# Performance work log

Measured on AMD Instinct MI355X. Metric: run time of the kernel, lower is better.

The kernel has to match this reference:

```python
import jax, jax.numpy as jnp
import numpy as np

N, E = 3200, 50000
RBF, HID = 16, 128
CUT = 5.0
NS, NV = 32, 16            # multiplicities of 0e and 1o blocks
D = NS + 3 * NV            # 80 = node/message irrep dim
WNUM = NS*NS + NV*NS + NS*NV + NV*NV  # 2304 tensor-product weights per edge
EPS = 1e-8
# path normalization (fully-connected TP, 2 paths per output irrep)
A1 = 1.0 / np.sqrt(2.0 * NS)
A2 = 1.0 / np.sqrt(2.0 * NV)
A3 = 1.0 / np.sqrt(2.0 * NS)
A4 = 1.0 / np.sqrt(2.0 * NV)
ISQ3 = 1.0 / np.sqrt(3.0)


def setup_inputs() -> dict:
    key = jax.random.key(0)
    ks = jax.random.split(key, 24)
    nrm = lambda k, s, sc=1.0: jax.random.normal(k, s, jnp.float32) * sc
    x = nrm(ks[0], (N, D))
    edge_src = jax.random.randint(ks[1], (E,), 0, N)
    edge_dst = jax.random.randint(ks[2], (E,), 0, N)
    dirs = nrm(ks[3], (E, 3))
    unit = dirs / jnp.linalg.norm(dirs, axis=1, keepdims=True)
    # component-normalized SH for l=0,1: [1, sqrt(3)*r_hat]
    edge_sh = jnp.concatenate([jnp.ones((E, 1), jnp.float32), np.sqrt(3.0) * unit], axis=1)
    edge_rbf = nrm(ks[4], (E, RBF))
    edge_len = jax.random.uniform(ks[5], (E,), jnp.float32, 0.1, 6.0)  # some beyond cutoff
    inp = dict(x=x, edge_src=edge_src, edge_dst=edge_dst, edge_sh=edge_sh,
               edge_rbf=edge_rbf, edge_len=edge_len)
    # IrrepNorm affine params
    inp['norm_w'] = jnp.ones((D,), jnp.float32)
    inp['norm_b'] = jnp.zeros((D,), jnp.float32)
    # radial weight MLP (RBF -> HID -> HID -> WNUM)
    inp['mw1'] = nrm(ks[6], (RBF, HID), 1.0/np.sqrt(RBF)); inp['mb1'] = jnp.zeros((HID,), jnp.float32)
    inp['mw2'] = nrm(ks[7], (HID, HID), 1.0/np.sqrt(HID)); inp['mb2'] = jnp.zeros((HID,), jnp.float32)
    inp['mw3'] = nrm(ks[8], (HID, WNUM), 1.0/np.sqrt(HID)); inp['mb3'] = jnp.zeros((WNUM,), jnp.float32)
    # edge gate MLP (RBF -> HID -> 1)
    inp['gw1'] = nrm(ks[9], (RBF, HID), 1.0/np.sqrt(RBF)); inp['gb1'] = jnp.zeros((HID,), jnp.float32)
    inp['gw2'] = nrm(ks[10], (HID, 1), 1.0/np.sqrt(HID)); inp['gb2'] = jnp.zeros((1,), jnp.float32)
    # equivariant linears (e3nn stores N(0,1) weights, normalizes by 1/sqrt(fan_in))
    inp['Ws'] = nrm(ks[11], (NS, NS + NV))   # msg_linear scalar part: 32 -> 32 scalars + 16 gates
    inp['Wv'] = nrm(ks[12], (NV, NV))        # msg_linear vector part
    inp['Us'] = nrm(ks[13], (NS, NS))        # update_linear
    inp['Uv'] = nrm(ks[14], (NV, NV))
    inp['Ss'] = nrm(ks[15], (NS, NS))        # self_linear
    inp['Sv'] = nrm(ks[16], (NV, NV))
    inp['res_scale'] = jnp.float32(0.1)
    return inp


def _irrep_norm(x, w, b):
    s = x[:, :NS]
    v = x[:, NS:].reshape(-1, NV, 3)
    mean = s.mean(axis=1, keepdims=True)
    var = ((s - mean) ** 2).mean(axis=1, keepdims=True)
    s = (s - mean) / jnp.sqrt(var + EPS)
    rms = jnp.sqrt((v ** 2).mean(axis=2, keepdims=True) + EPS)
    v = v / rms
    out = jnp.concatenate([s, v.reshape(-1, 3 * NV)], axis=-1)
    return out * w + b


def reference(x, edge_src, edge_dst, edge_sh, edge_rbf, edge_len,
              norm_w, norm_b, mw1, mb1, mw2, mb2, mw3, mb3,
              gw1, gb1, gw2, gb2, Ws, Wv, Us, Uv, Ss, Sv, res_scale):
    silu = jax.nn.silu
    x_norm = _irrep_norm(x, norm_w, norm_b)                  # [N, 80]
    # radial tensor-product weights per edge
    h = silu(edge_rbf @ mw1 + mb1)
    h = silu(h @ mw2 + mb2)
    tpw = h @ mw3 + mb3                                      # [E, 2304]
    o1 = NS*NS; o2 = o1 + NV*NS; o3 = o2 + NS*NV
    w1 = tpw[:, :o1].reshape(-1, NS, NS)
    w2 = tpw[:, o1:o2].reshape(-1, NV, NS)
    w3 = tpw[:, o2:o3].reshape(-1, NS, NV)
    w4 = tpw[:, o3:].reshape(-1, NV, NV)
    # gather source node features
    xs = x_norm[edge_src, :NS]                               # [E, 32]
    xv = x_norm[edge_src, NS:].reshape(-1, NV, 3)            # [E, 16, 3]
    sh0 = edge_sh[:, 0]                                      # [E]
    sh1 = edge_sh[:, 1:4]                                    # [E, 3]
    # fully-connected TP paths
    msg_s = A1 * jnp.einsum('ei,eio->eo', xs * sh0[:, None], w1)
    inner = jnp.einsum('eim,em->ei', xv, sh1) * ISQ3         # 1o x 1o -> 0e
    msg_s = msg_s + A2 * jnp.einsum('ei,eio->eo', inner, w2)
    msg_v = A3 * jnp.einsum('ei,eio->eo', xs, w3)[:, :, None] * sh1[:, None, :]
    msg_v = msg_v + A4 * jnp.einsum('eim,eio->eom', xv, w4) * sh0[:, None, None]
    m = jnp.concatenate([msg_s, msg_v.reshape(-1, 3 * NV)], axis=-1)  # [E, 80]
    # cutoff envelope and learned edge gate
    cutoff_w = 0.5 * (jnp.cos(jnp.pi * edge_len / CUT) + 1.0) * (edge_len <= CUT).astype(x.dtype)
    gate_w = jax.nn.sigmoid(silu(edge_rbf @ gw1 + gb1) @ gw2 + gb2)   # [E, 1]
    edge_w = cutoff_w[:, None] * gate_w                               # [E, 1]
    m = m * edge_w
    # scatter-add aggregate + normalization
    agg = jax.ops.segment_sum(m, edge_dst, num_segments=N)            # [N, 80]
    den = jax.ops.segment_sum(edge_w, edge_dst, num_segments=N)       # [N, 1]
    agg = agg / jnp.maximum(den, 1e-8)
    # msg_linear -> scalars + gates + gated vectors
    ag_s = agg[:, :NS]
    ag_v = agg[:, NS:].reshape(-1, NV, 3)
    sc = (ag_s @ Ws) / np.sqrt(NS)                                    # [N, 48]
    vc = jnp.einsum('nim,io->nom', ag_v, Wv) / np.sqrt(NV)            # [N, 16, 3]
    s_g = silu(sc[:, :NS])
    gates = jax.nn.sigmoid(sc[:, NS:])
    v_g = vc * gates[:, :, None]
    # update + self interaction
    upd_s = (s_g @ Us) / np.sqrt(NS)
    upd_v = jnp.einsum('nim,io->nom', v_g, Uv) / np.sqrt(NV)
    self_s = (x_norm[:, :NS] @ Ss) / np.sqrt(NS)
    self_v = jnp.einsum('nim,io->nom', x_norm[:, NS:].reshape(-1, NV, 3), Sv) / np.sqrt(NV)
    out = jnp.concatenate([self_s + upd_s, (self_v + upd_v).reshape(-1, 3 * NV)], axis=-1)
    return x + res_scale * out
```

## Files before the change

### kernel.cpp

```cpp
#include <hip/hip_runtime.h>
#include <hip/hip_bf16.h>
#include <math.h>

#define N_NODES 3200
#define E_EDGES 50000
#define RBFN 16
#define HID 128
#define NS 32
#define NV 16
#define DD 80
#define WNUM 2304
#define CUTF 5.0f
#define EPSF 1e-8f

#define A1C 0.125f
#define A2C 0.17677669529663687f
#define A3C 0.125f
#define A4C 0.17677669529663687f
#define A2ISQ 0.10206207261596575f

typedef __attribute__((ext_vector_type(4))) float f32x4;
typedef __attribute__((ext_vector_type(8))) short bf16x8;

__device__ __forceinline__ float sigm(float x) { return 1.0f / (1.0f + __expf(-x)); }
__device__ __forceinline__ float silu_f(float x) { return x * sigm(x); }

__device__ __forceinline__ short bf16r(float x) {
    union { float f; unsigned u; } v; v.f = x;
    unsigned r = (v.u + 0x7fffu + ((v.u >> 16) & 1u)) >> 16;
    return (short)r;
}
__device__ __forceinline__ float b2f(unsigned short s) {
    union { float f; unsigned u; } v; v.u = ((unsigned)s) << 16; return v.f;
}

__global__ void k_scan(const int* __restrict__ hist, int* __restrict__ start) {
    __shared__ int part[256];
    int t = threadIdx.x;
    int loc[13];
    int s = 0;
#pragma unroll
    for (int j = 0; j < 13; j++) {
        int idx = t * 13 + j;
        int v = (idx < N_NODES) ? hist[idx] : 0;
        loc[j] = s; s += v;
    }
    part[t] = s;
    __syncthreads();
    for (int off = 1; off < 256; off <<= 1) {
        int v = part[t];
        int add = (t >= off) ? part[t - off] : 0;
        __syncthreads();
        part[t] = v + add;
        __syncthreads();
    }
    int pre = (t == 0) ? 0 : part[t - 1];
#pragma unroll
    for (int j = 0; j < 13; j++) {
        int idx = t * 13 + j;
        if (idx < N_NODES) start[idx] = pre + loc[j];
    }
    if (t == 255) start[N_NODES] = part[255];
}

__global__ void k_scatter(const int* __restrict__ edst, const int* __restrict__ start,
                          int* __restrict__ cur, int* __restrict__ perm) {
    int e = blockIdx.x * 256 + threadIdx.x;
    if (e < E_EDGES) {
        int d = edst[e];
        int pos = start[d] + atomicAdd(&cur[d], 1);
        perm[pos] = e;
    }
}

__global__ void k_prep0(const float* __restrict__ mw2, __hip_bfloat16* __restrict__ mw2f) {
    __shared__ __hip_bfloat16 st[2048];
    int t = blockIdx.x, tid = threadIdx.x;
    for (int idx = tid; idx < 2048; idx += 256) {
        int k = idx >> 4, c = idx & 15;
        float v = mw2[k * HID + t * 16 + c];
        int kk = k >> 5, q4 = (k >> 3) & 3, j = k & 7;
        st[kk * 512 + (q4 * 16 + c) * 8 + j] = __float2bfloat16(v);
    }
    __syncthreads();
    ((bf16x8*)(mw2f + t * 2048))[tid] = ((const bf16x8*)st)[tid];
}

__global__ __launch_bounds__(256) void k_front(
    const float* __restrict__ rbf, const float* __restrict__ elen,
    const int* __restrict__ edst,
    const float* __restrict__ mw1, const float* __restrict__ mb1,
    const float* __restrict__ gw1, const float* __restrict__ gb1,
    const float* __restrict__ gw2, const float* __restrict__ gb2,
    const float* __restrict__ mb2, const __hip_bfloat16* __restrict__ mw2f,
    const float* __restrict__ mw3, const float* __restrict__ mb3,
    const float* __restrict__ x, const float* __restrict__ nw, const float* __restrict__ nb,
    float* __restrict__ ewg, __hip_bfloat16* __restrict__ h2b,
    __hip_bfloat16* __restrict__ mw3f, __hip_bfloat16* __restrict__ biasf,
    float* __restrict__ xn, int* __restrict__ hist) {
    __shared__ __align__(16) char smem[16640];
    int b = blockIdx.x, tid = threadIdx.x;
    if (b < 782) {
        __hip_bfloat16* h1l = (__hip_bfloat16*)smem;
        int wid = __builtin_amdgcn_readfirstlane(tid >> 6);
        int lane = tid & 63;
        int base = b * 64;
        int eb = base + wid * 16;
        {
            int c0 = lane, c1 = 64 + lane;
            float t0[16], t1[16], g0[16], g1[16];
            float b0 = mb1[c0], b1 = mb1[c1], gb0v = gb1[c0], gb1v = gb1[c1];
#pragma unroll
            for (int e = 0; e < 16; e++) { t0[e] = b0; t1[e] = b1; g0[e] = gb0v; g1[e] = gb1v; }
#pragma unroll
            for (int r = 0; r < RBFN; r++) {
                float w0 = mw1[r * HID + c0], w1 = mw1[r * HID + c1];
                float v0 = gw1[r * HID + c0], v1 = gw1[r * HID + c1];
#pragma unroll
                for (int e = 0; e < 16; e++) {
                    int ee = eb + e; if (ee >= E_EDGES) ee = E_EDGES - 1;
                    float rv = rbf[ee * RBFN + r];
                    t0[e] += rv * w0; t1[e] += rv * w1;
                    g0[e] += rv * v0; g1[e] += rv * v1;
                }
            }
            float q0 = gw2[c0], q1 = gw2[c1];
            float gb2v = gb2[0];
#pragma unroll
            for (int e = 0; e < 16; e++) {
                int le = wid * 16 + e;
                h1l[le * 128 + c0] = __float2bfloat16(silu_f(t0[e]));
                h1l[le * 128 + c1] = __float2bfloat16(silu_f(t1[e]));
                float p = silu_f(g0[e]) * q0 + silu_f(g1[e]) * q1;
                p += __shfl_xor(p, 1);  p += __shfl_xor(p, 2);  p += __shfl_xor(p, 4);
                p += __shfl_xor(p, 8);  p += __shfl_xor(p, 16); p += __shfl_xor(p, 32);
                if (lane == 0 && eb + e < E_EDGES) {
                    float len = elen[eb + e];
                    float cut = (len <= CUTF) ? 0.5f * (cosf(3.14159265358979f * len / CUTF) + 1.0f) : 0.f;
                    ewg[eb + e] = cut * sigm(p + gb2v);
                }
            }
        }
        __syncthreads();
        {
            int q4 = lane >> 4, l15 = lane & 15;
            int le = wid * 16 + l15;
            bf16x8 af[4];
#pragma unroll
            for (int kk = 0; kk < 4; kk++)
                af[kk] = *(const bf16x8*)(h1l + le * 128 + kk * 32 + q4 * 8);
            const f32x4 zf = {0.f, 0.f, 0.f, 0.f};
#pragma unroll
            for (int ct = 0; ct < 8; ct++) {
                f32x4 acc = zf;
#pragma unroll
                for (int kk = 0; kk < 4; kk++) {
                    bf16x8 bw = *(const bf16x8*)(mw2f + (ct * 4 + kk) * 512 + lane * 8);
                    acc = __builtin_amdgcn_mfma_f32_16x16x32_bf16(af[kk], bw, acc, 0, 0, 0);
                }
                float bias = mb2[ct * 16 + l15];
#pragma unroll
                for (int r = 0; r < 4; r++) {
                    int ge = base + wid * 16 + q4 * 4 + r;
                    if (ge < E_EDGES)
                        h2b[ge * HID + ct * 16 + l15] = __float2bfloat16(silu_f(acc[r] + bias));
                }
            }
        }
    } else if (b < 927) {
        int b2 = b - 782;
        __hip_bfloat16* st = (__hip_bfloat16*)smem;
        if (b2 < 144) {
            for (int idx = tid; idx < 2048; idx += 256) {
                int k = idx >> 4, c = idx & 15;
                float v = mw3[k * WNUM + b2 * 16 + c];
                int kk = k >> 5, q4 = (k >> 3) & 3, j = k & 7;
                st[kk * 512 + (q4 * 16 + c) * 8 + j] = __float2bfloat16(v);
            }
            __syncthreads();
            ((bf16x8*)(mw3f + b2 * 2048))[tid] = ((const bf16x8*)st)[tid];
        } else {
            for (int idx = tid; idx < 3072; idx += 256) {
                float val;
                if (idx < 1024) {
                    int oh = idx >> 9, l = (idx >> 3) & 63, j = idx & 7;
                    int o = oh * 16 + (l & 15), i = (l >> 4) * 8 + j;
                    val = mb3[i * 32 + o];
                } else if (idx < 2048) {
                    int t = idx - 1024;
                    int oh = t >> 9, l = (t >> 3) & 63, j = t & 7;
                    int o = oh * 16 + (l & 15), i = (l >> 4) * 8 + j;
                    val = (i < 16) ? mb3[1024 + i * 32 + o] : 0.f;
                } else if (idx < 2560) {
                    int t = idx - 2048;
                    int l = t >> 3, j = t & 7;
                    int o = l & 15, i = (l >> 4) * 8 + j;
                    val = mb3[1536 + i * 16 + o];
                } else {
                    int t = idx - 2560;
                    int l = t >> 3, j = t & 7;
                    int o = l & 15, i = (l >> 4) * 8 + j;
                    val = (i < 16) ? mb3[2048 + i * 16 + o] : 0.f;
                }
                biasf[idx] = __float2bfloat16(val);
            }
        }
    } else if (b < 1727) {
        float* row = (float*)smem;
        int sub = tid >> 6, t = tid & 63;
        int n = (b - 927) * 4 + sub;
        float* rw = row + sub * 80;
        const float* xr = x + n * DD;
        rw[t] = xr[t];
        if (t < 16) rw[64 + t] = xr[64 + t];
        __syncthreads();
        float mean = 0.f;
#pragma unroll
        for (int i = 0; i < NS; i++) mean += rw[i];
        mean *= (1.0f / NS);
        float var = 0.f;
#pragma unroll
        for (int i = 0; i < NS; i++) { float d = rw[i] - mean; var += d * d; }
        var *= (1.0f / NS);
        float inv = rsqrtf(var + EPSF);
        if (t < NS) xn[n * DD + t] = (rw[t] - mean) * inv * nw[t] + nb[t];
        if (t < 48) {
            int j = t / 3;
            float v0 = rw[NS + 3 * j], v1 = rw[NS + 3 * j + 1], v2 = rw[NS + 3 * j + 2];
            float rms = sqrtf((v0 * v0 + v1 * v1 + v2 * v2) * (1.0f / 3.0f) + EPSF);
            xn[n * DD + NS + t] = rw[NS + t] / rms * nw[NS + t] + nb[NS + t];
        }
    } else {
        int e = (b - 1727) * 256 + tid;
        if (e < E_EDGES) atomicAdd(&hist[edst[e]], 1);
    }
}

__global__ __launch_bounds__(128, 3) void k_msg(
    const float* __restrict__ xn, const __hip_bfloat16* __restrict__ h2b,
    const float* __restrict__ ewg, const int* __restrict__ esrc,
    const int* __restrict__ edst, const int* __restrict__ perm,
    const float* __restrict__ esh,
    const __hip_bfloat16* __restrict__ mw3f, const __hip_bfloat16* __restrict__ biasf,
    const int* __restrict__ startp, float* __restrict__ agg, float* __restrict__ agg2,
    float* __restrict__ den) {
    __shared__ __align__(16) char pool[29696];
    unsigned short (*xng)[82]  = (unsigned short(*)[82])(pool);
    unsigned short (*innr)[16] = (unsigned short(*)[16])(pool + 20992);
    float* sh0l = (float*)(pool + 25088);
    int* srcl   = (int*)(pool + 25600);
    int* gel    = (int*)(pool + 26112);
    int* dstl   = (int*)(pool + 26624);
    float* ewl  = (float*)(pool + 27136);
    float (*sh1l)[4] = (float(*)[4])(pool + 27648);
    float* msgl = (float*)pool;

    const int tid = threadIdx.x;
    const int wid = __builtin_amdgcn_readfirstlane(tid >> 6);
    const int lane = tid & 63;
    const int q4 = lane >> 4;
    const int l15 = lane & 15;
    const int ib = q4 * 8;
    const int grp = blockIdx.x / 5;
    const int slice = blockIdx.x - 5 * grp;
    const int e0 = grp * 128;

    {
        int slot = e0 + tid;
        bool v = slot < E_EDGES;
        int ge = v ? perm[slot] : 0;
        gel[tid] = ge;
        srcl[tid] = esrc[ge];
        dstl[tid] = v ? edst[ge] : -1;
        ewl[tid] = v ? ewg[ge] : 0.f;
        sh0l[tid] = esh[ge * 4];
        sh1l[tid][0] = esh[ge * 4 + 1];
        sh1l[tid][1] = esh[ge * 4 + 2];
        sh1l[tid][2] = esh[ge * 4 + 3];
    }
    __syncthreads();
    {
        int lo, hi;
        if (slice < 2)      { lo = 0;  hi = 32; }
        else if (slice < 4) { lo = 24; hi = 80; }
        else                { lo = 0;  hi = 80; }
        int nv4 = (hi - lo) >> 2;
        for (int idx = tid; idx < 128 * nv4; idx += 128) {
            int e = idx / nv4, k = idx - e * nv4;
            int q = lo + (k << 2);
            f32x4 v = *(const f32x4*)(xn + srcl[e] * 80 + q);
            unsigned p0 = ((unsigned)(unsigned short)bf16r(v[0])) |
                          (((unsigned)(unsigned short)bf16r(v[1])) << 16);
            unsigned p1 = ((unsigned)(unsigned short)bf16r(v[2])) |
                          (((unsigned)(unsigned short)bf16r(v[3])) << 16);
            unsigned* d = (unsigned*)&xng[e][q];
            d[0] = p0; d[1] = p1;
        }
    }
    __syncthreads();
    if (slice == 2 || slice == 3) {
        for (int idx = tid; idx < 128 * 16; idx += 128) {
            int e = idx >> 4, i = idx & 15;
            float d = b2f(xng[e][32 + 3 * i]) * sh1l[e][0]
                    + b2f(xng[e][32 + 3 * i + 1]) * sh1l[e][1]
                    + b2f(xng[e][32 + 3 * i + 2]) * sh1l[e][2];
            innr[e][i] = (unsigned short)bf16r(A2ISQ * d);
        }
        __syncthreads();
    }

    int el[4];
#pragma unroll
    for (int et = 0; et < 4; et++) el[et] = wid * 64 + et * 16 + l15;
    bf16x8 hfr[4][4];
#pragma unroll
    for (int et = 0; et < 4; et++) {
        int ge = gel[el[et]];
        const __hip_bfloat16* hr = h2b + ge * HID;
#pragma unroll
        for (int kk = 0; kk < 4; kk++)
            hfr[et][kk] = *(const bf16x8*)(hr + kk * 32 + ib);
    }
    const f32x4 zf = {0.f, 0.f, 0.f, 0.f};
    const bf16x8* gp = (const bf16x8*)mw3f;
    int cnt = E_EDGES - e0; if (cnt > 128) cnt = 128;

    if (slice < 4) {
        const int h = slice & 1;
        const int ch2 = slice >> 1;
        const int nlo = ch2 * 24, nhi = nlo + 24;
        float f1[4];
        f32x4 msgS[4];
#pragma unroll
        for (int et = 0; et < 4; et++) f1[et] = A1C * sh0l[el[et]];
#pragma unroll
        for (int et = 0; et < 4; et++) {
            bf16x8 pb;
            if (ch2 == 0) {
#pragma unroll
                for (int j = 0; j < 8; j++)
                    pb[j] = bf16r(b2f(xng[el[et]][ib + j]) * f1[et]);
            } else {
#pragma unroll
                for (int j = 0; j < 8; j++)
                    pb[j] = (ib + j < 16) ? (short)innr[el[et]][ib + j] : (short)0;
            }
            bf16x8 ba = *(const bf16x8*)(biasf + (ch2 * 1024 + h * 512) + lane * 8);
            msgS[et] = __builtin_amdgcn_mfma_f32_16x16x32_bf16(ba, pb, zf, 0, 0, 0);
        }
        auto computeS = [&](int n, bf16x8 (&A)[4]) {
            f32x4 acc[4];
#pragma unroll
            for (int et = 0; et < 4; et++) acc[et] = zf;
#pragma unroll
            for (int kk = 0; kk < 4; kk++)
#pragma unroll
                for (int et = 0; et < 4; et++)
                    acc[et] = __builtin_amdgcn_mfma_f32_16x16x32_bf16(
                        A[kk], hfr[et][kk], acc[et], 0, 0, 0);
            float p[4];
            if (n < 32) {
#pragma unroll
                for (int et = 0; et < 4; et++) p[et] = f1[et] * b2f(xng[el[et]][n]);
            } else {
#pragma unroll
                for (int et = 0; et < 4; et++) p[et] = b2f(innr[el[et]][n - 32]);
            }
#pragma unroll
            for (int et = 0; et < 4; et++)
#pragma unroll
                for (int r = 0; r < 4; r++)
                    msgS[et][r] += p[et] * acc[et][r];
        };
        bf16x8 A0[4], A1[4];
        {
            const bf16x8* g = gp + nlo * 512 + h * 256;
#pragma unroll
            for (int f = 0; f < 4; f++) A0[f] = g[f * 64 + lane];
        }
        for (int n = nlo; n < nhi; n += 2) {
            const bf16x8* g1 = gp + (n + 1) * 512 + h * 256;
#pragma unroll
            for (int f = 0; f < 4; f++) A1[f] = g1[f * 64 + lane];
            computeS(n, A0);
            if (n + 2 < nhi) {
                const bf16x8* g2 = gp + (n + 2) * 512 + h * 256;
#pragma unroll
                for (int f = 0; f < 4; f++) A0[f] = g2[f * 64 + lane];
            }
            computeS(n + 1, A1);
        }
        __syncthreads();
#pragma unroll
        for (int et = 0; et < 4; et++) {
            int le = el[et];
            float ew = ewl[le];
#pragma unroll
            for (int r = 0; r < 4; r++)
                msgl[le * 16 + q4 * 4 + r] = msgS[et][r] * ew;
        }
        __syncthreads();
        {
            int nch = (slice == 0) ? 17 : 16;
            int c = lane;
            int r0 = wid * 64;
            int rend = (cnt < r0 + 64) ? cnt : (r0 + 64);
            if (c < nch && r0 < cnt) {
                int cur = dstl[r0];
                float acc = 0.f;
                for (int r = r0; r < rend; r++) {
                    int nd = dstl[r];
                    if (nd != cur) {
                        if (cur >= 0) {
                            bool interior = (startp[cur] >= e0 + r0) && (startp[cur + 1] <= e0 + rend);
                            float* p = (c == 16) ? (den + cur)
                                     : ((slice == 0) ? (agg + cur * 80 + c)
                                     :  (slice == 1) ? (agg + cur * 80 + 16 + c)
                                     :  (slice == 2) ? (agg2 + cur * 32 + c)
                                                     : (agg2 + cur * 32 + 16 + c));
                            if (interior) *p = acc; else atomicAdd(p, acc);
                        }
                        acc = 0.f; cur = nd;
                    }
                    acc += (c == 16) ? ewl[r] : msgl[r * 16 + c];
                }
                if (cur >= 0) {
                    bool interior = (startp[cur] >= e0 + r0) && (startp[cur + 1] <= e0 + rend);
                    float* p = (c == 16) ? (den + cur)
                             : ((slice == 0) ? (agg + cur * 80 + c)
                             :  (slice == 1) ? (agg + cur * 80 + 16 + c)
                             :  (slice == 2) ? (agg2 + cur * 32 + c)
                                             : (agg2 + cur * 32 + 16 + c));
                    if (interior) *p = acc; else atomicAdd(p, acc);
                }
            }
        }
    } else {
        float f4e[4];
#pragma unroll
        for (int et = 0; et < 4; et++) f4e[et] = A4C * sh0l[el[et]];
        f32x4 q3[4];
#pragma unroll
        for (int et = 0; et < 4; et++) {
            bf16x8 xs8;
#pragma unroll
            for (int j = 0; j < 8; j++) xs8[j] = (short)xng[el[et]][ib + j];
            bf16x8 ba3 = *(const bf16x8*)(biasf + 2048 + lane * 8);
            q3[et] = __builtin_amdgcn_mfma_f32_16x16x32_bf16(ba3, xs8, zf, 0, 0, 0);
        }
        for (int n = 48; n < 64; ++n) {
            bf16x8 A[8];
            const bf16x8* g = gp + n * 512;
#pragma unroll
            for (int f = 0; f < 8; f++) A[f] = g[f * 64 + lane];
#pragma unroll
            for (int half = 0; half < 2; half++) {
                f32x4 acc[4];
#pragma unroll
                for (int et = 0; et < 4; et++) acc[et] = zf;
#pragma unroll
                for (int kk = 0; kk < 4; kk++)
#pragma unroll
                    for (int et = 0; et < 4; et++)
                        acc[et] = __builtin_amdgcn_mfma_f32_16x16x32_bf16(
                            A[half * 4 + kk], hfr[et][kk], acc[et], 0, 0, 0);
                int i = 2 * (n - 48) + half;
                float p[4];
#pragma unroll
                for (int et = 0; et < 4; et++) p[et] = b2f(xng[el[et]][i]);
#pragma unroll
                for (int et = 0; et < 4; et++)
#pragma unroll
                    for (int r = 0; r < 4; r++)
                        q3[et][r] += p[et] * acc[et][r];
            }
        }
        f32x4 qv[3][4];
#pragma unroll
        for (int et = 0; et < 4; et++) {
            bf16x8 ba4 = *(const bf16x8*)(biasf + 2560 + lane * 8);
#pragma unroll
            for (int m = 0; m < 3; m++) {
                bf16x8 t8;
#pragma unroll
                for (int j = 0; j < 8; j++) {
                    int i = ib + j;
                    t8[j] = (i < 16) ? (short)xng[el[et]][32 + 3 * i + m] : (short)0;
                }
                qv[m][et] = __builtin_amdgcn_mfma_f32_16x16x32_bf16(ba4, t8, zf, 0, 0, 0);
            }
        }
        for (int n = 64; n < 72; ++n) {
            bf16x8 A[8];
            const bf16x8* g = gp + n * 512;
#pragma unroll
            for (int f = 0; f < 8; f++) A[f] = g[f * 64 + lane];
#pragma unroll
            for (int half = 0; half < 2; half++) {
                f32x4 acc[4];
#pragma unroll
                for (int et = 0; et < 4; et++) acc[et] = zf;
#pragma unroll
                for (int kk = 0; kk < 4; kk++)
#pragma unroll
                    for (int et = 0; et < 4; et++)
                        acc[et] = __builtin_amdgcn_mfma_f32_16x16x32_bf16(
                            A[half * 4 + kk], hfr[et][kk], acc[et], 0, 0, 0);
                int i = 2 * (n - 64) + half;
#pragma unroll
                for (int m = 0; m < 3; m++) {
                    float p[4];
#pragma unroll
                    for (int et = 0; et < 4; et++) p[et] = b2f(xng[el[et]][32 + 3 * i + m]);
#pragma unroll
                    for (int et = 0; et < 4; et++)
#pragma unroll
                        for (int r = 0; r < 4; r++)
                            qv[m][et][r] += p[et] * acc[et][r];
                }
            }
        }
        __syncthreads();
#pragma unroll
        for (int et = 0; et < 4; et++) {
            int le = el[et];
            float ew = ewl[le];
            float s0 = sh1l[le][0], s1 = sh1l[le][1], s2 = sh1l[le][2];
            float b4 = f4e[et];
#pragma unroll
            for (int r = 0; r < 4; r++) {
                int o = q4 * 4 + r;
                float qq = A3C * q3[et][r];
                msgl[le * 48 + o * 3 + 0] = (qq * s0 + b4 * qv[0][et][r]) * ew;
                msgl[le * 48 + o * 3 + 1] = (qq * s1 + b4 * qv[1][et][r]) * ew;
                msgl[le * 48 + o * 3 + 2] = (qq * s2 + b4 * qv[2][et][r]) * ew;
            }
        }
        __syncthreads();
        {
            int c = lane;
            int r0 = wid * 64;
            int rend = (cnt < r0 + 64) ? cnt : (r0 + 64);
            if (c < 48 && r0 < cnt) {
                int cur = dstl[r0];
                float acc = 0.f;
                for (int r = r0; r < rend; r++) {
                    int nd = dstl[r];
                    if (nd != cur) {
                        if (cur >= 0) {
                            bool interior = (startp[cur] >= e0 + r0) && (startp[cur + 1] <= e0 + rend);
                            float* p = agg + cur * 80 + 32 + c;
                            if (interior) *p = acc; else atomicAdd(p, acc);
                        }
                        acc = 0.f; cur = nd;
                    }
                    acc += msgl[r * 48 + c];
                }
                if (cur >= 0) {
                    bool interior = (startp[cur] >= e0 + r0) && (startp[cur + 1] <= e0 + rend);
                    float* p = agg + cur * 80 + 32 + c;
                    if (interior) *p = acc; else atomicAdd(p, acc);
                }
            }
        }
    }
}

__global__ void k_update(
    const float* __restrict__ x, const float* __restrict__ xn,
    const float* __restrict__ agg, const float* __restrict__ agg2,
    const float* __restrict__ den,
    const float* __restrict__ Ws, const float* __restrict__ Wv,
    const float* __restrict__ Us, const float* __restrict__ Uv,
    const float* __restrict__ Ss, const float* __restrict__ Sv,
    const float* __restrict__ rsp, float* __restrict__ out) {
    int n = blockIdx.x, t = threadIdx.x;
    __shared__ float ag[DD];
    __shared__ float xnl[DD];
    __shared__ float sg[NS];
    __shared__ float gt[NV];
    __shared__ float vg[48];
    float idv = 1.0f / fmaxf(den[n], 1e-8f);
    float base = agg[n * DD + t];
    if (t < 32) base += agg2[n * 32 + t];
    ag[t] = base * idv;
    if (t < 16) ag[64 + t] = agg[n * DD + 64 + t] * idv;
    xnl[t] = xn[n * DD + t];
    if (t < 16) xnl[64 + t] = xn[n * DD + 64 + t];
    __syncthreads();
    const float iqs = 0.17677669529663687f;
    const float iqv = 0.25f;
    if (t < 48) {
        float acc = 0.f;
#pragma unroll
        for (int i = 0; i < NS; i++) acc += ag[i] * Ws[i * 48 + t];
        acc *= iqs;
        if (t < NS) sg[t] = silu_f(acc);
        else gt[t - NS] = sigm(acc);
    }
    __syncthreads();
    if (t < 48) {
        int o = t / 3, m = t - 3 * o;
        float acc = 0.f;
#pragma unroll
        for (int i = 0; i < NV; i++) acc += ag[NS + 3 * i + m] * Wv[i * NV + o];
        vg[t] = acc * iqv * gt[o];
    }
    __syncthreads();
    float rs = rsp[0];
    if (t < NS) {
        float us = 0.f, ss = 0.f;
#pragma unroll
        for (int i = 0; i < NS; i++) { us += sg[i] * Us[i * NS + t]; ss += xnl[i] * Ss[i * NS + t]; }
        out[n * DD + t] = x[n * DD + t] + rs * ((ss + us) * iqs);
    }
    if (t < 48) {
        int o = t / 3, m = t - 3 * o;
        float uv = 0.f, sv = 0.f;
#pragma unroll
        for (int i = 0; i < NV; i++) { uv += vg[3 * i + m] * Uv[i * NV + o]; sv += xnl[NS + 3 * i + m] * Sv[i * NV + o]; }
        out[n * DD + NS + t] = x[n * DD + NS + t] + rs * ((sv + uv) * iqv);
    }
}

extern "C" void kernel_launch(void* const* d_in, const int* in_sizes, int n_in,
                              void* d_out, int out_size, void* d_ws, size_t ws_size,
                              hipStream_t stream) {
    (void)in_sizes; (void)n_in; (void)out_size; (void)ws_size;
    const float* x    = (const float*)d_in[0];
    const int*   esrc = (const int*)d_in[1];
    const int*   edst = (const int*)d_in[2];
    const float* esh  = (const float*)d_in[3];
    const float* erbf = (const float*)d_in[4];
    const float* elen = (const float*)d_in[5];
    const float* nw   = (const float*)d_in[6];
    const float* nb   = (const float*)d_in[7];
    const float* mw1  = (const float*)d_in[8];
    const float* mb1  = (const float*)d_in[9];
    const float* mw2  = (const float*)d_in[10];
    const float* mb2  = (const float*)d_in[11];
    const float* mw3  = (const float*)d_in[12];
    const float* mb3  = (const float*)d_in[13];
    const float* gw1  = (const float*)d_in[14];
    const float* gb1  = (const float*)d_in[15];
    const float* gw2  = (const float*)d_in[16];
    const float* gb2  = (const float*)d_in[17];
    const float* Ws   = (const float*)d_in[18];
    const float* Wv   = (const float*)d_in[19];
    const float* Us   = (const float*)d_in[20];
    const float* Uv   = (const float*)d_in[21];
    const float* Ss   = (const float*)d_in[22];
    const float* Sv   = (const float*)d_in[23];
    const float* rsp  = (const float*)d_in[24];
    float* out = (float*)d_out;
    float* ws  = (float*)d_ws;

    float* agg    = ws;
    float* den    = ws + 256000;
    int*   hist   = (int*)(ws + 259200);
    int*   cur    = (int*)(ws + 262400);
    int*   startp = (int*)(ws + 265600);
    int*   perm   = (int*)(ws + 268801);
    float* xn     = ws + 318804;
    float* ewg    = ws + 574804;
    __hip_bfloat16* h2b   = (__hip_bfloat16*)(ws + 624804);
    __hip_bfloat16* mw3f  = (__hip_bfloat16*)(ws + 3824804);
    __hip_bfloat16* biasf = (__hip_bfloat16*)(ws + 3972260);
    __hip_bfloat16* mw2f  = (__hip_bfloat16*)(ws + 3973796);
    float* agg2   = ws + 3981988;

    hipMemsetAsync(ws, 0, 265600 * sizeof(float), stream);
    hipMemsetAsync(agg2, 0, 102400 * sizeof(float), stream);
    k_prep0<<<8, 256, 0, stream>>>(mw2, mw2f);
    k_front<<<1923, 256, 0, stream>>>(erbf, elen, edst, mw1, mb1, gw1, gb1, gw2, gb2,
                                      mb2, mw2f, mw3, mb3, x, nw, nb,
                                      ewg, h2b, mw3f, biasf, xn, hist);
    k_scan<<<1, 256, 0, stream>>>(hist, startp);
    k_scatter<<<196, 256, 0, stream>>>(edst, startp, cur, perm);
    k_msg<<<1955, 128, 0, stream>>>(xn, h2b, ewg, esrc, edst, perm, esh,
                                    mw3f, biasf, startp, agg, agg2, den);
    k_update<<<N_NODES, 64, 0, stream>>>(x, xn, agg, agg2, den, Ws, Wv, Us, Uv, Ss, Sv, rsp, out);
}
```

Before: 262.9 us.

## Pre-permute edge data by destination and store h2 in MFMA-tiled layout

The CSR build (histogram, scan, scatter) now runs before the front kernel. The scatter writes dst, src and sh arrays already in sorted order along with an inverse permutation. The front kernel writes edge weights and the h2 activations directly into sorted positions, with h2 in a 16-edge tiled layout that matches the MFMA fragment loads in the message kernel. It also emits a bf16 copy of the normalized node features, so the message kernel loads them with 16-byte vector reads instead of converting from fp32. This removes the gather through perm and the fp32→bf16 conversion from the hot message kernel. The cost is scattered writes in the front kernel, a serialized CSR build ahead of the front kernel, and launch bounds loosened from 3 to 2 blocks per unit, which may reduce occupancy.

```diff
diff --git a/kernel.cpp b/kernel.cpp
--- a/kernel.cpp
+++ b/kernel.cpp
@@ -34,6 +34,11 @@
     union { float f; unsigned u; } v; v.u = ((unsigned)s) << 16; return v.f;
 }
 
+__global__ void k_hist(const int* __restrict__ edst, int* __restrict__ hist) {
+    int e = blockIdx.x * 256 + threadIdx.x;
+    if (e < E_EDGES) atomicAdd(&hist[edst[e]], 1);
+}
+
 __global__ void k_scan(const int* __restrict__ hist, int* __restrict__ start) {
     __shared__ int part[256];
     int t = threadIdx.x;
@@ -63,13 +68,20 @@
     if (t == 255) start[N_NODES] = part[255];
 }
 
-__global__ void k_scatter(const int* __restrict__ edst, const int* __restrict__ start,
-                          int* __restrict__ cur, int* __restrict__ perm) {
+__global__ void k_scatter(const int* __restrict__ edst, const int* __restrict__ esrc,
+                          const float* __restrict__ esh, const int* __restrict__ start,
+                          int* __restrict__ cur, int* __restrict__ inv,
+                          int* __restrict__ edstp, int* __restrict__ esrcp,
+                          float* __restrict__ eshp) {
     int e = blockIdx.x * 256 + threadIdx.x;
     if (e < E_EDGES) {
         int d = edst[e];
         int pos = start[d] + atomicAdd(&cur[d], 1);
-        perm[pos] = e;
+        inv[e] = pos;
+        edstp[pos] = d;
+        esrcp[pos] = esrc[e];
+        f32x4 s = *(const f32x4*)(esh + e * 4);
+        *(f32x4*)(eshp + pos * 4) = s;
     }
 }
 
@@ -88,20 +100,21 @@
 
 __global__ __launch_bounds__(256) void k_front(
     const float* __restrict__ rbf, const float* __restrict__ elen,
-    const int* __restrict__ edst,
+    const int* __restrict__ inv,
     const float* __restrict__ mw1, const float* __restrict__ mb1,
     const float* __restrict__ gw1, const float* __restrict__ gb1,
     const float* __restrict__ gw2, const float* __restrict__ gb2,
     const float* __restrict__ mb2, const __hip_bfloat16* __restrict__ mw2f,
     const float* __restrict__ mw3, const float* __restrict__ mb3,
     const float* __restrict__ x, const float* __restrict__ nw, const float* __restrict__ nb,
-    float* __restrict__ ewg, __hip_bfloat16* __restrict__ h2b,
+    float* __restrict__ ewg, unsigned short* __restrict__ h2p,
     __hip_bfloat16* __restrict__ mw3f, __hip_bfloat16* __restrict__ biasf,
-    float* __restrict__ xn, int* __restrict__ hist) {
+    float* __restrict__ xn, unsigned short* __restrict__ xnb) {
     __shared__ __align__(16) char smem[16640];
     int b = blockIdx.x, tid = threadIdx.x;
     if (b < 782) {
         __hip_bfloat16* h1l = (__hip_bfloat16*)smem;
+        float* gatep = (float*)(smem + 16384);
         int wid = __builtin_amdgcn_readfirstlane(tid >> 6);
         int lane = tid & 63;
         int base = b * 64;
@@ -134,14 +147,18 @@
                 float p = silu_f(g0[e]) * q0 + silu_f(g1[e]) * q1;
                 p += __shfl_xor(p, 1);  p += __shfl_xor(p, 2);  p += __shfl_xor(p, 4);
                 p += __shfl_xor(p, 8);  p += __shfl_xor(p, 16); p += __shfl_xor(p, 32);
-                if (lane == 0 && eb + e < E_EDGES) {
-                    float len = elen[eb + e];
-                    float cut = (len <= CUTF) ? 0.5f * (cosf(3.14159265358979f * len / CUTF) + 1.0f) : 0.f;
-                    ewg[eb + e] = cut * sigm(p + gb2v);
-                }
-            }
-        }
-        __syncthreads();
+                if (lane == 0) gatep[le] = p + gb2v;
+            }
+        }
+        __syncthreads();
+        if (lane < 16) {
+            int ee = eb + lane;
+            if (ee < E_EDGES) {
+                float len = elen[ee];
+                float cut = (len <= CUTF) ? 0.5f * (cosf(3.14159265358979f * len / CUTF) + 1.0f) : 0.f;
+                ewg[inv[ee]] = cut * sigm(gatep[wid * 16 + lane]);
+            }
+        }
         {
             int q4 = lane >> 4, l15 = lane & 15;
             int le = wid * 16 + l15;
@@ -149,6 +166,12 @@
 #pragma unroll
             for (int kk = 0; kk < 4; kk++)
                 af[kk] = *(const bf16x8*)(h1l + le * 128 + kk * 32 + q4 * 8);
+            int pos4[4];
+#pragma unroll
+            for (int r = 0; r < 4; r++) {
+                int ge = base + wid * 16 + q4 * 4 + r;
+                pos4[r] = (ge < E_EDGES) ? inv[ge] : -1;
+            }
             const f32x4 zf = {0.f, 0.f, 0.f, 0.f};
 #pragma unroll
             for (int ct = 0; ct < 8; ct++) {
@@ -159,11 +182,14 @@
                     acc = __builtin_amdgcn_mfma_f32_16x16x32_bf16(af[kk], bw, acc, 0, 0, 0);
                 }
                 float bias = mb2[ct * 16 + l15];
+                int c = ct * 16 + l15;
+                int f = c >> 3, j = c & 7;
 #pragma unroll
                 for (int r = 0; r < 4; r++) {
-                    int ge = base + wid * 16 + q4 * 4 + r;
-                    if (ge < E_EDGES)
-                        h2b[ge * HID + ct * 16 + l15] = __float2bfloat16(silu_f(acc[r] + bias));
+                    int pos = pos4[r];
+                    if (pos >= 0)
+                        h2p[(pos >> 4) * 2048 + f * 128 + (pos & 15) * 8 + j] =
+                            (unsigned short)bf16r(silu_f(acc[r] + bias));
                 }
             }
         }
@@ -205,7 +231,7 @@
                 biasf[idx] = __float2bfloat16(val);
             }
         }
-    } else if (b < 1727) {
+    } else {
         float* row = (float*)smem;
         int sub = tid >> 6, t = tid & 63;
         int n = (b - 927) * 4 + sub;
@@ -222,37 +248,38 @@
 #pragma unroll
         for (int i = 0; i < NS; i++) { float d = rw[i] - mean; var += d * d; }
         var *= (1.0f / NS);
-        float inv = rsqrtf(var + EPSF);
-        if (t < NS) xn[n * DD + t] = (rw[t] - mean) * inv * nw[t] + nb[t];
+        float inv_ = rsqrtf(var + EPSF);
+        if (t < NS) {
+            float v = (rw[t] - mean) * inv_ * nw[t] + nb[t];
+            xn[n * DD + t] = v;
+            xnb[n * DD + t] = (unsigned short)bf16r(v);
+        }
         if (t < 48) {
             int j = t / 3;
             float v0 = rw[NS + 3 * j], v1 = rw[NS + 3 * j + 1], v2 = rw[NS + 3 * j + 2];
             float rms = sqrtf((v0 * v0 + v1 * v1 + v2 * v2) * (1.0f / 3.0f) + EPSF);
-            xn[n * DD + NS + t] = rw[NS + t] / rms * nw[NS + t] + nb[NS + t];
-        }
-    } else {
-        int e = (b - 1727) * 256 + tid;
-        if (e < E_EDGES) atomicAdd(&hist[edst[e]], 1);
-    }
-}
-
-__global__ __launch_bounds__(128, 3) void k_msg(
-    const float* __restrict__ xn, const __hip_bfloat16* __restrict__ h2b,
-    const float* __restrict__ ewg, const int* __restrict__ esrc,
-    const int* __restrict__ edst, const int* __restrict__ perm,
-    const float* __restrict__ esh,
+            float v = rw[NS + t] / rms * nw[NS + t] + nb[NS + t];
+            xn[n * DD + NS + t] = v;
+            xnb[n * DD + NS + t] = (unsigned short)bf16r(v);
+        }
+    }
+}
+
+__global__ __launch_bounds__(128, 2) void k_msg(
+    const unsigned short* __restrict__ xnb, const unsigned short* __restrict__ h2p,
+    const float* __restrict__ ewg, const int* __restrict__ edstp,
+    const int* __restrict__ esrcp, const float* __restrict__ eshp,
     const __hip_bfloat16* __restrict__ mw3f, const __hip_bfloat16* __restrict__ biasf,
     const int* __restrict__ startp, float* __restrict__ agg, float* __restrict__ agg2,
     float* __restrict__ den) {
-    __shared__ __align__(16) char pool[29696];
-    unsigned short (*xng)[82]  = (unsigned short(*)[82])(pool);
-    unsigned short (*innr)[16] = (unsigned short(*)[16])(pool + 20992);
-    float* sh0l = (float*)(pool + 25088);
-    int* srcl   = (int*)(pool + 25600);
-    int* gel    = (int*)(pool + 26112);
-    int* dstl   = (int*)(pool + 26624);
-    float* ewl  = (float*)(pool + 27136);
-    float (*sh1l)[4] = (float(*)[4])(pool + 27648);
+    __shared__ __align__(16) char pool[30720];
+    unsigned short (*xng)[88]  = (unsigned short(*)[88])(pool);
+    unsigned short (*innr)[16] = (unsigned short(*)[16])(pool + 22528);
+    float* sh0l = (float*)(pool + 26624);
+    int* srcl   = (int*)(pool + 27136);
+    int* dstl   = (int*)(pool + 27648);
+    float* ewl  = (float*)(pool + 28160);
+    float (*sh1l)[4] = (float(*)[4])(pool + 28672);
     float* msgl = (float*)pool;
 
     const int tid = threadIdx.x;
@@ -268,33 +295,29 @@
     {
         int slot = e0 + tid;
         bool v = slot < E_EDGES;
-        int ge = v ? perm[slot] : 0;
-        gel[tid] = ge;
-        srcl[tid] = esrc[ge];
-        dstl[tid] = v ? edst[ge] : -1;
-        ewl[tid] = v ? ewg[ge] : 0.f;
-        sh0l[tid] = esh[ge * 4];
-        sh1l[tid][0] = esh[ge * 4 + 1];
-        sh1l[tid][1] = esh[ge * 4 + 2];
-        sh1l[tid][2] = esh[ge * 4 + 3];
+        dstl[tid] = v ? edstp[slot] : -1;
+        srcl[tid] = v ? esrcp[slot] : 0;
+        ewl[tid]  = v ? ewg[slot] : 0.f;
+        f32x4 s = {0.f, 0.f, 0.f, 0.f};
+        if (v) s = *(const f32x4*)(eshp + slot * 4);
+        sh0l[tid] = s[0];
+        sh1l[tid][0] = s[1]; sh1l[tid][1] = s[2]; sh1l[tid][2] = s[3];
     }
     __syncthreads();
-    {
-        int lo, hi;
-        if (slice < 2)      { lo = 0;  hi = 32; }
-        else if (slice < 4) { lo = 24; hi = 80; }
-        else                { lo = 0;  hi = 80; }
-        int nv4 = (hi - lo) >> 2;
-        for (int idx = tid; idx < 128 * nv4; idx += 128) {
-            int e = idx / nv4, k = idx - e * nv4;
-            int q = lo + (k << 2);
-            f32x4 v = *(const f32x4*)(xn + srcl[e] * 80 + q);
-            unsigned p0 = ((unsigned)(unsigned short)bf16r(v[0])) |
-                          (((unsigned)(unsigned short)bf16r(v[1])) << 16);
-            unsigned p1 = ((unsigned)(unsigned short)bf16r(v[2])) |
-                          (((unsigned)(unsigned short)bf16r(v[3])) << 16);
-            unsigned* d = (unsigned*)&xng[e][q];
-            d[0] = p0; d[1] = p1;
+    if (slice < 2) {
+        for (int idx = tid; idx < 128 * 4; idx += 128) {
+            int e = idx >> 2, q = (idx & 3) * 8;
+            *(bf16x8*)&xng[e][q] = *(const bf16x8*)(xnb + srcl[e] * 80 + q);
+        }
+    } else if (slice < 4) {
+        for (int idx = tid; idx < 128 * 7; idx += 128) {
+            int e = idx / 7, q = 24 + (idx - e * 7) * 8;
+            *(bf16x8*)&xng[e][q] = *(const bf16x8*)(xnb + srcl[e] * 80 + q);
+        }
+    } else {
+        for (int idx = tid; idx < 128 * 10; idx += 128) {
+            int e = idx / 10, q = (idx - e * 10) * 8;
+            *(bf16x8*)&xng[e][q] = *(const bf16x8*)(xnb + srcl[e] * 80 + q);
         }
     }
     __syncthreads();
@@ -312,14 +335,14 @@
     int el[4];
 #pragma unroll
     for (int et = 0; et < 4; et++) el[et] = wid * 64 + et * 16 + l15;
+    const int tbase = (e0 >> 4) + wid * 4;
     bf16x8 hfr[4][4];
 #pragma unroll
     for (int et = 0; et < 4; et++) {
-        int ge = gel[el[et]];
-        const __hip_bfloat16* hr = h2b + ge * HID;
+        const unsigned short* tp = h2p + (tbase + et) * 2048;
 #pragma unroll
         for (int kk = 0; kk < 4; kk++)
-            hfr[et][kk] = *(const bf16x8*)(hr + kk * 32 + ib);
+            hfr[et][kk] = *(const bf16x8*)(tp + (kk * 4 + q4) * 128 + l15 * 8);
     }
     const f32x4 zf = {0.f, 0.f, 0.f, 0.f};
     const bf16x8* gp = (const bf16x8*)mw3f;
@@ -660,24 +683,30 @@
     int*   hist   = (int*)(ws + 259200);
     int*   cur    = (int*)(ws + 262400);
     int*   startp = (int*)(ws + 265600);
-    int*   perm   = (int*)(ws + 268801);
+    int*   inv    = (int*)(ws + 268801);
     float* xn     = ws + 318804;
     float* ewg    = ws + 574804;
-    __hip_bfloat16* h2b   = (__hip_bfloat16*)(ws + 624804);
-    __hip_bfloat16* mw3f  = (__hip_bfloat16*)(ws + 3824804);
-    __hip_bfloat16* biasf = (__hip_bfloat16*)(ws + 3972260);
-    __hip_bfloat16* mw2f  = (__hip_bfloat16*)(ws + 3973796);
-    float* agg2   = ws + 3981988;
+    unsigned short* h2p = (unsigned short*)(ws + 624804);
+    __hip_bfloat16* mw3f  = (__hip_bfloat16*)(ws + 3827876);
+    __hip_bfloat16* biasf = (__hip_bfloat16*)(ws + 3975332);
+    __hip_bfloat16* mw2f  = (__hip_bfloat16*)(ws + 3976868);
+    float* agg2   = ws + 3985060;
+    int* edstp    = (int*)(ws + 4087460);
+    int* esrcp    = (int*)(ws + 4137508);
+    float* eshp   = ws + 4187556;
+    unsigned short* xnb = (unsigned short*)(ws + 4387748);
 
     hipMemsetAsync(ws, 0, 265600 * sizeof(float), stream);
     hipMemsetAsync(agg2, 0, 102400 * sizeof(float), stream);
+    k_hist<<<196, 256, 0, stream>>>(edst, hist);
+    k_scan<<<1, 256, 0, stream>>>(hist, startp);
+    k_scatter<<<196, 256, 0, stream>>>(edst, esrc, esh, startp, cur,
+                                       inv, edstp, esrcp, eshp);
     k_prep0<<<8, 256, 0, stream>>>(mw2, mw2f);
-    k_front<<<1923, 256, 0, stream>>>(erbf, elen, edst, mw1, mb1, gw1, gb1, gw2, gb2,
+    k_front<<<1727, 256, 0, stream>>>(erbf, elen, inv, mw1, mb1, gw1, gb1, gw2, gb2,
                                       mb2, mw2f, mw3, mb3, x, nw, nb,
-                                      ewg, h2b, mw3f, biasf, xn, hist);
-    k_scan<<<1, 256, 0, stream>>>(hist, startp);
-    k_scatter<<<196, 256, 0, stream>>>(edst, startp, cur, perm);
-    k_msg<<<1955, 128, 0, stream>>>(xn, h2b, ewg, esrc, edst, perm, esh,
+                                      ewg, h2p, mw3f, biasf, xn, xnb);
+    k_msg<<<1955, 128, 0, stream>>>(xnb, h2p, ewg, edstp, esrcp, eshp,
                                     mw3f, biasf, startp, agg, agg2, den);
     k_update<<<N_NODES, 64, 0, stream>>>(x, xn, agg, agg2, den, Ws, Wv, Us, Uv, Ss, Sv, rsp, out);
 }
```

New measurement: 240.7 us. 8.5% less time.
